# Kernel tuning notes

Measured on AMD Instinct MI355X. Metric: run time of the kernel, lower is better.

Reference implementation:

```python
import jax, jax.numpy as jnp
import numpy as np

TROPICAL_ZERO = jnp.float32(-1e38)  # tropical additive identity (acts as -inf)


def setup_inputs() -> dict:
    key = jax.random.key(0)
    k_x, k_w = jax.random.split(key)
    B, IN, OUT = 4096, 256, 256
    x = jax.random.normal(k_x, (B, IN), dtype=jnp.float32)
    # weight = log(rand + 1e-6), matching nn.Parameter init in the torch module
    weight = jnp.log(jax.random.uniform(k_w, (OUT, IN), dtype=jnp.float32) + 1e-6)
    bias = jnp.zeros((OUT,), dtype=jnp.float32)
    return {"x": x, "weight": weight, "bias": bias}


def reference(x, weight, bias):
    # Tropical (max-plus) matmul: out[b, j] = max_k (x[b, k] + w[j, k]) + bias[j]
    # restricted to 'non-tropical-zero' products; if all products are tropical
    # zero, the output stays TROPICAL_ZERO (no bias added), as in the torch loop.
    products = x[:, None, :] + weight[None, :, :]          # [B, out, in]
    mask = products > TROPICAL_ZERO                        # [B, out, in]
    masked = jnp.where(mask, products, -jnp.inf)
    max_val = jnp.max(masked, axis=-1)                     # [B, out]
    any_valid = jnp.any(mask, axis=-1)                     # [B, out]
    out = jnp.where(any_valid, max_val + bias[None, :], TROPICAL_ZERO)
    return out
```

## Files before the change

### kernel.cpp

```cpp
#include <hip/hip_runtime.h>


#define TZERO -1e38f

constexpr int K    = 256;
constexpr int N    = 256;
constexpr int RPW  = 8;
constexpr int WAVES = 4;
constexpr int BM   = RPW * WAVES;
constexpr int BN   = 64;
constexpr int NT   = 64 * WAVES;

__global__ __launch_bounds__(NT, 2)
void tropical_kernel(const float* __restrict__ x, const float* __restrict__ w,
                     const float* __restrict__ bias, float* __restrict__ out)
{
    __shared__ float4 wQ[64][64];

    const int t    = threadIdx.x;
    const int row0 = blockIdx.x * BM;
    const int col0 = blockIdx.y * BN;

#pragma unroll
    for (int i = 0; i < (64 * 64) / NT; ++i) {
        const int flat = t + i * NT;
        const int j    = flat & 63;
        const int k4   = flat >> 6;
        wQ[k4][j] = *reinterpret_cast<const float4*>(
            w + (size_t)(col0 + j) * K + k4 * 4);
    }
    __syncthreads();

    const int lane = t & 63;
    const int wave = __builtin_amdgcn_readfirstlane(t >> 6);
    const float* xw = x + (size_t)(row0 + wave * RPW) * K;

    float acc[RPW];
#pragma unroll
    for (int r = 0; r < RPW; ++r) acc[r] = -__builtin_inff();

#pragma unroll 4
    for (int k4 = 0; k4 < K / 4; ++k4) {
        const float4 wv = wQ[k4][lane];
#pragma unroll
        for (int r = 0; r < RPW; ++r) {
            const float4 xv = *reinterpret_cast<const float4*>(xw + r * K + k4 * 4);
            const float t0 = xv.x + wv.x;
            const float t1 = xv.y + wv.y;
            const float t2 = xv.z + wv.z;
            const float t3 = xv.w + wv.w;
            float m = fmaxf(fmaxf(acc[r], t0), t1);
            m       = fmaxf(fmaxf(m, t2), t3);
            acc[r] = m;
        }
    }

    const float bj = bias[col0 + lane];
    float* orow = out + (size_t)(row0 + wave * RPW) * N + col0 + lane;
#pragma unroll
    for (int r = 0; r < RPW; ++r) {
        const float v = acc[r];
        orow[(size_t)r * N] = (v > TZERO) ? v + bj : TZERO;
    }
}

extern "C" void kernel_launch(void* const* d_in, const int* in_sizes, int n_in,
                              void* d_out, int out_size, void* d_ws, size_t ws_size,
                              hipStream_t stream) {
    const float* x  = (const float*)d_in[0];
    const float* w  = (const float*)d_in[1];
    const float* b  = (const float*)d_in[2];
    float* out      = (float*)d_out;

    dim3 grid(4096 / BM, N / BN);
    tropical_kernel<<<grid, NT, 0, stream>>>(x, w, b, out);
}
```

Baseline: 76.90 us.

## Double-buffer weight tiles in K chunks and halve rows per wave

Splits the K dimension into 64-wide chunks and double-buffers the weight tile in LDS, loading the next chunk while computing the current one. Rows per wave drop from 8 to 4, so the grid has twice as many blocks, and launch bounds now ask for 4 blocks per CU. The aim is to cut LDS footprint, raise occupancy and hide the up-front weight load latency. In exchange it adds a barrier per chunk and halves reuse of each weight read from LDS, giving more LDS traffic per FLOP.

```diff
diff --git a/kernel.cpp b/kernel.cpp
--- a/kernel.cpp
+++ b/kernel.cpp
@@ -3,60 +3,76 @@
 
 #define TZERO -1e38f
 
-constexpr int K    = 256;
-constexpr int N    = 256;
-constexpr int RPW  = 8;
+constexpr int K     = 256;
+constexpr int N     = 256;
+constexpr int RPW   = 4;
 constexpr int WAVES = 4;
-constexpr int BM   = RPW * WAVES;
-constexpr int BN   = 64;
-constexpr int NT   = 64 * WAVES;
+constexpr int BM    = RPW * WAVES;
+constexpr int BN    = 64;
+constexpr int NT    = 64 * WAVES;
+constexpr int BK    = 64;
+constexpr int NC    = K / BK;
+constexpr int K4C   = BK / 4;
 
-__global__ __launch_bounds__(NT, 2)
+__global__ __launch_bounds__(NT, 4)
 void tropical_kernel(const float* __restrict__ x, const float* __restrict__ w,
                      const float* __restrict__ bias, float* __restrict__ out)
 {
-    __shared__ float4 wQ[64][64];
+    __shared__ float4 wQ[2][K4C][BN];
 
     const int t    = threadIdx.x;
-    const int row0 = blockIdx.x * BM;
+    const int lane = t & 63;
+    const int wave = __builtin_amdgcn_readfirstlane(t >> 6);
+    const int row0 = blockIdx.x * BM + wave * RPW;
     const int col0 = blockIdx.y * BN;
 
+    const int scol = t & 63;
+    const int sq   = t >> 6;
+    const float* wsrc = w + (size_t)(col0 + scol) * K + sq * 16;
+
 #pragma unroll
-    for (int i = 0; i < (64 * 64) / NT; ++i) {
-        const int flat = t + i * NT;
-        const int j    = flat & 63;
-        const int k4   = flat >> 6;
-        wQ[k4][j] = *reinterpret_cast<const float4*>(
-            w + (size_t)(col0 + j) * K + k4 * 4);
-    }
+    for (int i = 0; i < 4; ++i)
+        wQ[0][sq * 4 + i][scol] =
+            *reinterpret_cast<const float4*>(wsrc + i * 4);
     __syncthreads();
 
-    const int lane = t & 63;
-    const int wave = __builtin_amdgcn_readfirstlane(t >> 6);
-    const float* xw = x + (size_t)(row0 + wave * RPW) * K;
+    const float* xw = x + (size_t)row0 * K;
 
     float acc[RPW];
 #pragma unroll
     for (int r = 0; r < RPW; ++r) acc[r] = -__builtin_inff();
 
-#pragma unroll 4
-    for (int k4 = 0; k4 < K / 4; ++k4) {
-        const float4 wv = wQ[k4][lane];
+    for (int c = 0; c < NC; ++c) {
+        if (c + 1 < NC) {
+            const float* ws = wsrc + (c + 1) * BK;
 #pragma unroll
-        for (int r = 0; r < RPW; ++r) {
-            const float4 xv = *reinterpret_cast<const float4*>(xw + r * K + k4 * 4);
-            const float t0 = xv.x + wv.x;
-            const float t1 = xv.y + wv.y;
-            const float t2 = xv.z + wv.z;
-            const float t3 = xv.w + wv.w;
-            float m = fmaxf(fmaxf(acc[r], t0), t1);
-            m       = fmaxf(fmaxf(m, t2), t3);
-            acc[r] = m;
+            for (int i = 0; i < 4; ++i)
+                wQ[(c + 1) & 1][sq * 4 + i][scol] =
+                    *reinterpret_cast<const float4*>(ws + i * 4);
         }
+
+        const float* xc = xw + c * BK;
+#pragma unroll 8
+        for (int k4 = 0; k4 < K4C; ++k4) {
+            const float4 wv = wQ[c & 1][k4][lane];
+#pragma unroll
+            for (int r = 0; r < RPW; ++r) {
+                const float4 xv =
+                    *reinterpret_cast<const float4*>(xc + r * K + k4 * 4);
+                const float t0 = xv.x + wv.x;
+                const float t1 = xv.y + wv.y;
+                const float t2 = xv.z + wv.z;
+                const float t3 = xv.w + wv.w;
+                float m = fmaxf(fmaxf(acc[r], t0), t1);
+                m       = fmaxf(fmaxf(m, t2), t3);
+                acc[r] = m;
+            }
+        }
+        __syncthreads();
     }
 
     const float bj = bias[col0 + lane];
-    float* orow = out + (size_t)(row0 + wave * RPW) * N + col0 + lane;
+    float* orow = out + (size_t)row0 * N + col0 + lane;
 #pragma unroll
     for (int r = 0; r < RPW; ++r) {
         const float v = acc[r];
```

Result: faster. 72.97 us (-5.1%).

## Keep weight slice in registers and split K across waves with LDS reduction

Applied to the files above, without the earlier changes.

Each wave now holds a 64-wide K-quarter of its column's weights in registers instead of staging the full weight tile in LDS. The four waves split the K dimension, and their partial maxima are combined through a small shared-memory reduction. Each block covers 16 rows, giving more blocks, and launch bounds target higher occupancy. This removes the per-iteration LDS weight reads, but needs 64 extra registers per thread and adds a reduction step with a barrier. Weight reuse per block also drops, so global weight loads increase.

```diff
diff --git a/kernel.cpp b/kernel.cpp
--- a/kernel.cpp
+++ b/kernel.cpp
@@ -3,64 +3,73 @@
 
 #define TZERO -1e38f
 
-constexpr int K    = 256;
-constexpr int N    = 256;
-constexpr int RPW  = 8;
+constexpr int K     = 256;
+constexpr int N     = 256;
+constexpr int Bdim  = 4096;
+constexpr int BN    = 64;
+constexpr int RPB   = 16;
 constexpr int WAVES = 4;
-constexpr int BM   = RPW * WAVES;
-constexpr int BN   = 64;
-constexpr int NT   = 64 * WAVES;
+constexpr int KQ    = K / WAVES;
+constexpr int NT    = 64 * WAVES;
 
-__global__ __launch_bounds__(NT, 2)
+__global__ __launch_bounds__(NT, 4)
 void tropical_kernel(const float* __restrict__ x, const float* __restrict__ w,
                      const float* __restrict__ bias, float* __restrict__ out)
 {
-    __shared__ float4 wQ[64][64];
+    __shared__ float red[WAVES][RPB][BN];
 
     const int t    = threadIdx.x;
-    const int row0 = blockIdx.x * BM;
+    const int lane = t & 63;
+    const int wave = __builtin_amdgcn_readfirstlane(t >> 6);
+    const int row0 = blockIdx.x * RPB;
     const int col0 = blockIdx.y * BN;
 
+    float wr[KQ];
+    {
+        const float* wp = w + (size_t)(col0 + lane) * K + wave * KQ;
 #pragma unroll
-    for (int i = 0; i < (64 * 64) / NT; ++i) {
-        const int flat = t + i * NT;
-        const int j    = flat & 63;
-        const int k4   = flat >> 6;
-        wQ[k4][j] = *reinterpret_cast<const float4*>(
-            w + (size_t)(col0 + j) * K + k4 * 4);
-    }
-    __syncthreads();
-
-    const int lane = t & 63;
-    const int wave = __builtin_amdgcn_readfirstlane(t >> 6);
-    const float* xw = x + (size_t)(row0 + wave * RPW) * K;
-
-    float acc[RPW];
-#pragma unroll
-    for (int r = 0; r < RPW; ++r) acc[r] = -__builtin_inff();
-
-#pragma unroll 4
-    for (int k4 = 0; k4 < K / 4; ++k4) {
-        const float4 wv = wQ[k4][lane];
-#pragma unroll
-        for (int r = 0; r < RPW; ++r) {
-            const float4 xv = *reinterpret_cast<const float4*>(xw + r * K + k4 * 4);
-            const float t0 = xv.x + wv.x;
-            const float t1 = xv.y + wv.y;
-            const float t2 = xv.z + wv.z;
-            const float t3 = xv.w + wv.w;
-            float m = fmaxf(fmaxf(acc[r], t0), t1);
-            m       = fmaxf(fmaxf(m, t2), t3);
-            acc[r] = m;
+        for (int i4 = 0; i4 < KQ / 4; ++i4) {
+            const float4 v = *reinterpret_cast<const float4*>(wp + i4 * 4);
+            wr[i4 * 4 + 0] = v.x;
+            wr[i4 * 4 + 1] = v.y;
+            wr[i4 * 4 + 2] = v.z;
+            wr[i4 * 4 + 3] = v.w;
         }
     }
 
-    const float bj = bias[col0 + lane];
-    float* orow = out + (size_t)(row0 + wave * RPW) * N + col0 + lane;
+    const float* xq = x + (size_t)row0 * K + wave * KQ;
+
+    float acc[RPB];
+#pragma unroll 1
+    for (int r = 0; r < RPB; ++r) {
+        const float* xr = xq + (size_t)r * K;
+        float m = -__builtin_inff();
 #pragma unroll
-    for (int r = 0; r < RPW; ++r) {
-        const float v = acc[r];
-        orow[(size_t)r * N] = (v > TZERO) ? v + bj : TZERO;
+        for (int i4 = 0; i4 < KQ / 4; ++i4) {
+            const float4 xv = *reinterpret_cast<const float4*>(xr + i4 * 4);
+            const float t0 = xv.x + wr[i4 * 4 + 0];
+            const float t1 = xv.y + wr[i4 * 4 + 1];
+            const float t2 = xv.z + wr[i4 * 4 + 2];
+            const float t3 = xv.w + wr[i4 * 4 + 3];
+            m = fmaxf(fmaxf(m, t0), t1);
+            m = fmaxf(fmaxf(m, t2), t3);
+        }
+        acc[r] = m;
+    }
+
+#pragma unroll
+    for (int r = 0; r < RPB; ++r) red[wave][r][lane] = acc[r];
+    __syncthreads();
+
+    const int rbase = wave * (RPB / WAVES);
+    const float bj  = bias[col0 + lane];
+#pragma unroll
+    for (int i = 0; i < RPB / WAVES; ++i) {
+        const int r = rbase + i;
+        const float m = fmaxf(fmaxf(red[0][r][lane], red[1][r][lane]),
+                              fmaxf(red[2][r][lane], red[3][r][lane]));
+        out[(size_t)(row0 + r) * N + col0 + lane] =
+            (m > TZERO) ? m + bj : TZERO;
     }
 }
 
@@ -72,6 +81,6 @@
     const float* b  = (const float*)d_in[2];
     float* out      = (float*)d_out;
 
-    dim3 grid(4096 / BM, N / BN);
+    dim3 grid(Bdim / RPB, N / BN);
     tropical_kernel<<<grid, NT, 0, stream>>>(x, w, b, out);
 }
```

Result: slower. 94.67 us (+23.1%).

## Split K across waves with shared-memory max reduction and smaller row tiles

Applied to the files above, without the earlier changes.

Changes the block to 512 threads covering 16 rows by 64 columns, with the K dimension split into four chunks handled by separate waves. Partial maxima go to shared memory, reusing the weight tile buffer, and are combined before the bias and store. The weight staging loop is also reorganised so each thread loads 8 contiguous float4s per column. The goal is more parallelism and more waves per block so latency is better hidden. The cost is extra syncs and a reduction pass, and each weight tile is now reused across fewer rows, so weights are reloaded more often.

```diff
diff --git a/kernel.cpp b/kernel.cpp
--- a/kernel.cpp
+++ b/kernel.cpp
@@ -5,46 +5,53 @@
 
 constexpr int K    = 256;
 constexpr int N    = 256;
-constexpr int RPW  = 8;
-constexpr int WAVES = 4;
-constexpr int BM   = RPW * WAVES;
+constexpr int Bdim = 4096;
 constexpr int BN   = 64;
-constexpr int NT   = 64 * WAVES;
+constexpr int BM   = 16;
+constexpr int RPT  = 8;
+constexpr int NKC  = 4;
+constexpr int KC   = K / NKC;
+constexpr int NT   = 512;
 
-__global__ __launch_bounds__(NT, 2)
+__global__ __launch_bounds__(NT, 4)
 void tropical_kernel(const float* __restrict__ x, const float* __restrict__ w,
                      const float* __restrict__ bias, float* __restrict__ out)
 {
-    __shared__ float4 wQ[64][64];
+    __shared__ float4 wQ[K / 4][BN];
+    float* red = reinterpret_cast<float*>(wQ);
 
     const int t    = threadIdx.x;
+    const int lane = t & 63;
     const int row0 = blockIdx.x * BM;
     const int col0 = blockIdx.y * BN;
 
+    {
+        const int scol = t & 63;
+        const int k8   = t >> 6;
+        const float* wp = w + (size_t)(col0 + scol) * K + k8 * 32;
 #pragma unroll
-    for (int i = 0; i < (64 * 64) / NT; ++i) {
-        const int flat = t + i * NT;
-        const int j    = flat & 63;
-        const int k4   = flat >> 6;
-        wQ[k4][j] = *reinterpret_cast<const float4*>(
-            w + (size_t)(col0 + j) * K + k4 * 4);
+        for (int i = 0; i < 8; ++i)
+            wQ[k8 * 8 + i][scol] = *reinterpret_cast<const float4*>(wp + i * 4);
     }
     __syncthreads();
 
-    const int lane = t & 63;
-    const int wave = __builtin_amdgcn_readfirstlane(t >> 6);
-    const float* xw = x + (size_t)(row0 + wave * RPW) * K;
+    const int wid = t >> 6;
+    const int rg  = wid & 1;
+    const int kc  = wid >> 1;
 
-    float acc[RPW];
+    const float* xp = x + (size_t)(row0 + rg * RPT) * K + kc * KC;
+
+    float acc[RPT];
 #pragma unroll
-    for (int r = 0; r < RPW; ++r) acc[r] = -__builtin_inff();
+    for (int r = 0; r < RPT; ++r) acc[r] = -__builtin_inff();
 
-#pragma unroll 4
-    for (int k4 = 0; k4 < K / 4; ++k4) {
-        const float4 wv = wQ[k4][lane];
 #pragma unroll
-        for (int r = 0; r < RPW; ++r) {
-            const float4 xv = *reinterpret_cast<const float4*>(xw + r * K + k4 * 4);
+    for (int k4 = 0; k4 < KC / 4; ++k4) {
+        const float4 wv = wQ[kc * (KC / 4) + k4][lane];
+#pragma unroll
+        for (int r = 0; r < RPT; ++r) {
+            const float4 xv =
+                *reinterpret_cast<const float4*>(xp + r * K + k4 * 4);
             const float t0 = xv.x + wv.x;
             const float t1 = xv.y + wv.y;
             const float t2 = xv.z + wv.z;
@@ -55,12 +62,21 @@
         }
     }
 
+    __syncthreads();
+#pragma unroll
+    for (int r = 0; r < RPT; ++r)
+        red[(kc * BM + rg * RPT + r) * BN + lane] = acc[r];
+    __syncthreads();
+
     const float bj = bias[col0 + lane];
-    float* orow = out + (size_t)(row0 + wave * RPW) * N + col0 + lane;
 #pragma unroll
-    for (int r = 0; r < RPW; ++r) {
-        const float v = acc[r];
-        orow[(size_t)r * N] = (v > TZERO) ? v + bj : TZERO;
+    for (int i = 0; i < 2; ++i) {
+        const int row = wid * 2 + i;
+        float m = red[(0 * BM + row) * BN + lane];
+        m = fmaxf(m, red[(1 * BM + row) * BN + lane]);
+        m = fmaxf(m, red[(2 * BM + row) * BN + lane]);
+        m = fmaxf(m, red[(3 * BM + row) * BN + lane]);
+        out[(size_t)(row0 + row) * N + col0 + lane] = (m > TZERO) ? m + bj : TZERO;
     }
 }
 
@@ -72,6 +88,6 @@
     const float* b  = (const float*)d_in[2];
     float* out      = (float*)d_out;
 
-    dim3 grid(4096 / BM, N / BN);
+    dim3 grid(Bdim / BM, N / BN);
     tropical_kernel<<<grid, NT, 0, stream>>>(x, w, b, out);
 }
```

Result: slower. 95.80 us (+24.6%).
